# Kernel optimization log

Measured on AMD Instinct MI355X. Metric: run time of the kernel, lower is better.

The kernel has to match this reference:

```python
import jax, jax.numpy as jnp
import numpy as np

D_MODEL = 2048
N_HEADS = 16
HEAD_DIM = D_MODEL // N_HEADS
FF = 8192
KCONV = 4
EPS = 1e-5


def _layernorm(x, w, b, eps=EPS):
    m = jnp.mean(x, axis=-1, keepdims=True)
    v = jnp.mean(jnp.square(x - m), axis=-1, keepdims=True)
    return (x - m) * jax.lax.rsqrt(v + eps) * w + b


def setup_inputs() -> dict:
    key = jax.random.key(0)
    ks = jax.random.split(key, 32)
    B, T = 2, 4096
    s = lambda fan: 1.0 / np.sqrt(fan)
    inp = {
        "x": jax.random.normal(ks[0], (B, T, D_MODEL), jnp.float32),
        # attention projections (stored as [in, out])
        "Wq": jax.random.normal(ks[1], (D_MODEL, D_MODEL), jnp.float32) * s(D_MODEL),
        "Wk": jax.random.normal(ks[2], (D_MODEL, D_MODEL), jnp.float32) * s(D_MODEL),
        "Wv": jax.random.normal(ks[3], (D_MODEL, D_MODEL), jnp.float32) * s(D_MODEL),
        "Wo": jax.random.normal(ks[4], (D_MODEL, D_MODEL), jnp.float32) * s(D_MODEL),
        # depthwise causal conv (torch Conv1d weight layout [C,1,K])
        "conv_w": jax.random.normal(ks[5], (D_MODEL, 1, KCONV), jnp.float32) * s(KCONV),
        "conv_b": jnp.zeros((D_MODEL,), jnp.float32),
        # gates (matching reset_parameters: zero weights, special biases)
        "Wig": jnp.zeros((D_MODEL, D_MODEL), jnp.float32),
        "big": jnp.full((D_MODEL,), -3.0, jnp.float32),
        "Wog": jax.random.normal(ks[6], (D_MODEL, D_MODEL), jnp.float32) * s(D_MODEL),
        "bog": jnp.zeros((D_MODEL,), jnp.float32),
        "Wg": jnp.zeros((D_MODEL, N_HEADS), jnp.float32),
        "bg": jnp.asarray(np.log(
            (lambda d: d / (1.0 - d))(
                1.0 - np.exp(np.linspace(np.log(1 - 0.9), np.log(1 - 0.999), N_HEADS))
            )
        ), jnp.float32),
        # norms
        "vnw": jnp.ones((HEAD_DIM,), jnp.float32),
        "vnb": jnp.zeros((HEAD_DIM,), jnp.float32),
        "mnw": jnp.ones((HEAD_DIM,), jnp.float32),
        "mnb": jnp.zeros((HEAD_DIM,), jnp.float32),
        "gnw": jnp.ones((D_MODEL,), jnp.float32),
        "gnb": jnp.zeros((D_MODEL,), jnp.float32),
        "ln1w": jnp.ones((D_MODEL,), jnp.float32),
        "ln1b": jnp.zeros((D_MODEL,), jnp.float32),
        "ln2w": jnp.ones((D_MODEL,), jnp.float32),
        "ln2b": jnp.zeros((D_MODEL,), jnp.float32),
        # SwiGLU MLP
        "Wgate": jax.random.normal(ks[7], (D_MODEL, FF), jnp.float32) * s(D_MODEL),
        "Wval": jax.random.normal(ks[8], (D_MODEL, FF), jnp.float32) * s(D_MODEL),
        "Wout": jax.random.normal(ks[9], (FF, D_MODEL), jnp.float32) * s(FF),
    }
    return inp


def _long_block(x, Wq, Wk, Wv, Wo, conv_w, conv_b, Wig, big, Wog, bog, Wg, bg,
                vnw, vnb, mnw, mnb, gnw, gnb, ln1w, ln1b, ln2w, ln2b,
                Wgate, Wval, Wout):
    B, T, C = x.shape
    H, D = N_HEADS, HEAD_DIM

    # ---- ln1 + LongAttention ----
    h = _layernorm(x, ln1w, ln1b)

    # depthwise causal conv over time
    ht = jnp.transpose(h, (0, 2, 1))  # [B, C, T]
    xc = jax.lax.conv_general_dilated(
        ht, conv_w, window_strides=(1,), padding=[(KCONV - 1, 0)],
        dimension_numbers=("NCH", "OIH", "NCH"), feature_group_count=C,
    ) + conv_b[None, :, None]
    x_conv = jax.nn.silu(jnp.transpose(xc, (0, 2, 1)))  # [B, T, C]

    def l2norm(t):
        return t * jax.lax.rsqrt(jnp.sum(t * t, axis=-1, keepdims=True) + 1e-12)

    q = l2norm((h @ Wq).reshape(B, T, H, D))
    k = l2norm((h @ Wk).reshape(B, T, H, D))
    v = _layernorm((h @ Wv).reshape(B, T, H, D), vnw, vnb)

    i_gate = jax.nn.sigmoid(x_conv @ Wig + big).reshape(B, T, H, D)
    gamma = jax.nn.sigmoid(x_conv @ Wg + bg).reshape(B, T, H, 1)

    # gated linear-attention recurrence: mem_t = gamma_t * mem_{t-1} + i_t * k_t * v_t
    u = i_gate * k * v
    g = jnp.broadcast_to(gamma, u.shape)

    def combine(c1, c2):
        a1, b1 = c1
        a2, b2 = c2
        return (a1 * a2, a2 * b1 + b2)

    _, mem = jax.lax.associative_scan(combine, (g, u), axis=1)  # [B, T, H, D]

    out = (_layernorm(mem, mnw, mnb) * q).reshape(B, T, C)

    # GroupNorm(num_heads, d_model) applied per token
    og = out.reshape(B, T, H, D)
    m = jnp.mean(og, axis=-1, keepdims=True)
    var = jnp.mean(jnp.square(og - m), axis=-1, keepdims=True)
    og = (og - m) * jax.lax.rsqrt(var + EPS)
    out = (og * gnw.reshape(H, D) + gnb.reshape(H, D)).reshape(B, T, C)

    out = out * jax.nn.sigmoid(x_conv @ Wog + bog)
    h = x + out @ Wo

    # ---- ln2 + SwiGLU MLP ----
    h2 = _layernorm(h, ln2w, ln2b)
    mlp = (jax.nn.silu(h2 @ Wgate) * (h2 @ Wval)) @ Wout
    return h + mlp


def reference(x, Wq, Wk, Wv, Wo, conv_w, conv_b, Wig, big, Wog, bog, Wg, bg,
              vnw, vnb, mnw, mnb, gnw, gnb, ln1w, ln1b, ln2w, ln2b,
              Wgate, Wval, Wout):
    return _long_block(x, Wq, Wk, Wv, Wo, conv_w, conv_b, Wig, big, Wog, bog,
                       Wg, bg, vnw, vnb, mnw, mnb, gnw, gnb, ln1w, ln1b,
                       ln2w, ln2b, Wgate, Wval, Wout)
```

## Files before the change

kernel.cpp:

```cpp
#include <hip/hip_runtime.h>


#define D_MODEL 2048
#define NHEADS 16
#define HEADDIM 128
#define FFDIM 8192
#define BSZ 2
#define TLEN 4096
#define MTOK (BSZ * TLEN)
#define CHUNK 128
#define NCHUNK (TLEN / CHUNK)

typedef unsigned short u16;
typedef __attribute__((ext_vector_type(8))) short bf16x8;
typedef __attribute__((ext_vector_type(4))) float f32x4;

__device__ __forceinline__ float bf2f(unsigned u) {
    u <<= 16;
    float f;
    __builtin_memcpy(&f, &u, 4);
    return f;
}
__device__ __forceinline__ u16 f2bf(float f) {
    unsigned u;
    __builtin_memcpy(&u, &f, 4);
    u = u + 0x7fffu + ((u >> 16) & 1u);
    return (u16)(u >> 16);
}
__device__ __forceinline__ void unpack8(uint4 p, float* v) {
    v[0] = bf2f(p.x & 0xffffu); v[1] = bf2f(p.x >> 16);
    v[2] = bf2f(p.y & 0xffffu); v[3] = bf2f(p.y >> 16);
    v[4] = bf2f(p.z & 0xffffu); v[5] = bf2f(p.z >> 16);
    v[6] = bf2f(p.w & 0xffffu); v[7] = bf2f(p.w >> 16);
}
__device__ __forceinline__ uint4 pack8(const float* v) {
    uint4 p;
    p.x = (unsigned)f2bf(v[0]) | ((unsigned)f2bf(v[1]) << 16);
    p.y = (unsigned)f2bf(v[2]) | ((unsigned)f2bf(v[3]) << 16);
    p.z = (unsigned)f2bf(v[4]) | ((unsigned)f2bf(v[5]) << 16);
    p.w = (unsigned)f2bf(v[6]) | ((unsigned)f2bf(v[7]) << 16);
    return p;
}
__device__ __forceinline__ float sigmoidf_(float x) { return 1.0f / (1.0f + __expf(-x)); }

__device__ __forceinline__ float ld1f(const void* p, size_t i, int f) {
    return f ? ((const float*)p)[i] : bf2f(((const u16*)p)[i]);
}
__device__ __forceinline__ void ld8f(const void* p, size_t i, int f, float* v) {
    if (f) {
        const float4* fp = (const float4*)((const float*)p + i);
        float4 a = fp[0], b = fp[1];
        v[0] = a.x; v[1] = a.y; v[2] = a.z; v[3] = a.w;
        v[4] = b.x; v[5] = b.y; v[6] = b.z; v[7] = b.w;
    } else {
        uint4 q = *(const uint4*)((const u16*)p + i);
        unpack8(q, v);
    }
}

__device__ __forceinline__ void async16(const u16* g, u16* l) {
    __builtin_amdgcn_global_load_lds((const __attribute__((address_space(1))) void*)g,
                                     (__attribute__((address_space(3))) void*)l, 16, 0, 0);
}

__global__ __launch_bounds__(256) void detect_k(const u16* __restrict__ probe, int* __restrict__ flag) {
    int tid = threadIdx.x;
    int cnt = 0;
    for (int i = tid; i < 16384; i += 256) {
        unsigned e = (probe[i] >> 7) & 0xFFu;
        if (e == 0xFFu) cnt++;
    }
#pragma unroll
    for (int off = 32; off; off >>= 1) cnt += __shfl_xor(cnt, off, 64);
    __shared__ int tot[4];
    if ((tid & 63) == 0) tot[tid >> 6] = cnt;
    __syncthreads();
    if (tid == 0) flag[0] = (tot[0] + tot[1] + tot[2] + tot[3] > 4) ? 1 : 0;
}

__global__ void copyflag_k(const int* __restrict__ a, int* __restrict__ b) { b[0] = a[0]; }

__global__ __launch_bounds__(256) void transpose_k(const void* __restrict__ in, u16* __restrict__ out,
                                                   int K, int N, const int* __restrict__ fl) {
    int f = *fl;
    __shared__ u16 tile[32][33];
    int n0 = blockIdx.x * 32, k0 = blockIdx.y * 32;
    int tx = threadIdx.x, ty = threadIdx.y;
#pragma unroll
    for (int j = 0; j < 4; ++j)
        tile[ty + j * 8][tx] = f2bf(ld1f(in, (size_t)(k0 + ty + j * 8) * N + n0 + tx, f));
    __syncthreads();
#pragma unroll
    for (int j = 0; j < 4; ++j)
        out[(size_t)(n0 + ty + j * 8) * K + k0 + tx] = tile[tx][ty + j * 8];
}

template <int IN_RAW>
__global__ __launch_bounds__(256) void ln_rows(const void* __restrict__ in, u16* __restrict__ out,
                                               const void* __restrict__ w, const void* __restrict__ bb,
                                               const int* __restrict__ fl) {
    int f = *fl;
    int m = blockIdx.x, tid = threadIdx.x;
    size_t base = (size_t)m * D_MODEL + tid * 8;
    float v[8];
    ld8f(in, base, IN_RAW ? f : 0, v);
    float s = 0.f, ss = 0.f;
#pragma unroll
    for (int i = 0; i < 8; ++i) { s += v[i]; ss += v[i] * v[i]; }
#pragma unroll
    for (int off = 32; off; off >>= 1) { s += __shfl_xor(s, off, 64); ss += __shfl_xor(ss, off, 64); }
    __shared__ float red[8];
    int lane = tid & 63, wvi = tid >> 6;
    if (lane == 0) { red[wvi] = s; red[4 + wvi] = ss; }
    __syncthreads();
    s = red[0] + red[1] + red[2] + red[3];
    ss = red[4] + red[5] + red[6] + red[7];
    float mu = s * (1.f / D_MODEL);
    float var = ss * (1.f / D_MODEL) - mu * mu;
    float rs = rsqrtf(var + 1e-5f);
    int ci = tid * 8;
    float o[8];
#pragma unroll
    for (int i = 0; i < 8; ++i)
        o[i] = (v[i] - mu) * rs * ld1f(w, ci + i, f) + ld1f(bb, ci + i, f);
    *(uint4*)&out[base] = pack8(o);
}

__global__ __launch_bounds__(256) void conv_silu_k(const u16* __restrict__ h, const void* __restrict__ cw,
                                                   const void* __restrict__ cb, u16* __restrict__ out,
                                                   const int* __restrict__ fl) {
    int f = *fl;
    int m = blockIdx.x, tid = threadIdx.x;
    int b = m >> 12, t = m & (TLEN - 1);
    int c = tid * 8;
    float acc[8];
#pragma unroll
    for (int i = 0; i < 8; ++i) acc[i] = ld1f(cb, c + i, f);
    float wv[8][4];
#pragma unroll
    for (int i = 0; i < 8; ++i) {
        if (f) {
            float4 wp = *(const float4*)((const float*)cw + (size_t)(c + i) * 4);
            wv[i][0] = wp.x; wv[i][1] = wp.y; wv[i][2] = wp.z; wv[i][3] = wp.w;
        } else {
            uint2 wp = *(const uint2*)((const u16*)cw + (size_t)(c + i) * 4);
            wv[i][0] = bf2f(wp.x & 0xffffu); wv[i][1] = bf2f(wp.x >> 16);
            wv[i][2] = bf2f(wp.y & 0xffffu); wv[i][3] = bf2f(wp.y >> 16);
        }
    }
#pragma unroll
    for (int j = 0; j < 4; ++j) {
        int tj = t - 3 + j;
        if (tj < 0) continue;
        uint4 hp = *(const uint4*)&h[((size_t)(b * TLEN + tj)) * D_MODEL + c];
        float hv[8];
        unpack8(hp, hv);
#pragma unroll
        for (int i = 0; i < 8; ++i) acc[i] += wv[i][j] * hv[i];
    }
    float o[8];
#pragma unroll
    for (int i = 0; i < 8; ++i) o[i] = acc[i] * sigmoidf_(acc[i]);
    *(uint4*)&out[(size_t)m * D_MODEL + c] = pack8(o);
}

template <int EPI>
__global__ __launch_bounds__(256) void gemm_bt(const u16* __restrict__ A, const u16* __restrict__ BT,
                                               void* out, const void* aux, const int* fl,
                                               long long oofs, int M, int N, int K) {
    __shared__ u16 As[128 * 32];
    __shared__ u16 Bs[128 * 32];
    const int tid = threadIdx.x;
    const int lane = tid & 63;
    const int wv = tid >> 6;
    const int m0 = blockIdx.y * 128, n0 = blockIdx.x * 128;
    const int wm = (wv >> 1) * 64, wn = (wv & 1) * 64;

    const int c0 = tid, c1 = tid + 256;
    const u16* Ag0 = A + (size_t)(m0 + (c0 >> 2)) * K + ((c0 & 3) * 8);
    const u16* Ag1 = A + (size_t)(m0 + (c1 >> 2)) * K + ((c1 & 3) * 8);
    const u16* Bg0 = BT + (size_t)(n0 + (c0 >> 2)) * K + ((c0 & 3) * 8);
    const u16* Bg1 = BT + (size_t)(n0 + (c1 >> 2)) * K + ((c1 & 3) * 8);
    u16* lA0 = &As[wv * 512];
    u16* lA1 = &As[2048 + wv * 512];
    u16* lB0 = &Bs[wv * 512];
    u16* lB1 = &Bs[2048 + wv * 512];

    f32x4 acc[4][4];
#pragma unroll
    for (int i = 0; i < 4; ++i)
#pragma unroll
        for (int j = 0; j < 4; ++j) acc[i][j] = (f32x4)0.0f;

    const int arow = (lane & 15) * 32 + (lane >> 4) * 8;
    const int kit = K >> 5;
    for (int kt = 0; kt < kit; ++kt) {
        __syncthreads();
        async16(Ag0, lA0);
        async16(Ag1, lA1);
        async16(Bg0, lB0);
        async16(Bg1, lB1);
        Ag0 += 32; Ag1 += 32; Bg0 += 32; Bg1 += 32;
        __syncthreads();
        bf16x8 af[4], bfr[4];
#pragma unroll
        for (int i = 0; i < 4; ++i) af[i] = *(const bf16x8*)&As[(wm + i * 16) * 32 + arow];
#pragma unroll
        for (int j = 0; j < 4; ++j) bfr[j] = *(const bf16x8*)&Bs[(wn + j * 16) * 32 + arow];
#pragma unroll
        for (int i = 0; i < 4; ++i)
#pragma unroll
            for (int j = 0; j < 4; ++j)
                acc[i][j] = __builtin_amdgcn_mfma_f32_16x16x32_bf16(af[i], bfr[j], acc[i][j], 0, 0, 0);
    }

    int f = (EPI == 1 || EPI == 2 || EPI == 4) ? *fl : 0;
    const int col0 = n0 + wn + (lane & 15);
    const int row0 = m0 + wm + ((lane >> 4) << 2);
#pragma unroll
    for (int i = 0; i < 4; ++i) {
#pragma unroll
        for (int r = 0; r < 4; ++r) {
            int row = row0 + i * 16 + r;
            size_t base = (size_t)row * N;
#pragma unroll
            for (int j = 0; j < 4; ++j) {
                int col = col0 + j * 16;
                float v = acc[i][j][r];
                if (EPI == 0) {
                    ((u16*)out)[base + col] = f2bf(v);
                } else if (EPI == 1) {
                    ((u16*)out)[base + col] = f2bf(sigmoidf_(v + ld1f(aux, col, f)));
                } else if (EPI == 2) {
                    ((u16*)out)[base + col] = f2bf(v + ld1f(aux, base + col, f));
                } else if (EPI == 3) {
                    float g = bf2f(((const u16*)aux)[base + col]);
                    ((u16*)out)[base + col] = f2bf(g * sigmoidf_(g) * v);
                } else {
                    float hr = bf2f(((const u16*)aux)[base + col]);
                    if (f) ((float*)out)[oofs + base + col] = v + hr;
                    else   ((u16*)out)[oofs + base + col] = f2bf(v + hr);
                }
            }
        }
    }
}

__global__ __launch_bounds__(256) void l2norm_k(u16* __restrict__ x) {
    int m = blockIdx.x, tid = threadIdx.x;
    size_t base = (size_t)m * D_MODEL + tid * 8;
    uint4 p = *(const uint4*)&x[base];
    float v[8];
    unpack8(p, v);
    float s = 0.f;
#pragma unroll
    for (int i = 0; i < 8; ++i) s += v[i] * v[i];
    s += __shfl_xor(s, 1, 64); s += __shfl_xor(s, 2, 64);
    s += __shfl_xor(s, 4, 64); s += __shfl_xor(s, 8, 64);
    float sc = rsqrtf(s + 1e-12f);
    float o[8];
#pragma unroll
    for (int i = 0; i < 8; ++i) o[i] = v[i] * sc;
    *(uint4*)&x[base] = pack8(o);
}

__global__ __launch_bounds__(256) void vnorm_k(u16* __restrict__ x, const void* __restrict__ w,
                                               const void* __restrict__ bb, const int* __restrict__ fl) {
    int f = *fl;
    int m = blockIdx.x, tid = threadIdx.x;
    size_t base = (size_t)m * D_MODEL + tid * 8;
    uint4 p = *(const uint4*)&x[base];
    float v[8];
    unpack8(p, v);
    float s = 0.f, ss = 0.f;
#pragma unroll
    for (int i = 0; i < 8; ++i) { s += v[i]; ss += v[i] * v[i]; }
    s += __shfl_xor(s, 1, 64); s += __shfl_xor(s, 2, 64);
    s += __shfl_xor(s, 4, 64); s += __shfl_xor(s, 8, 64);
    ss += __shfl_xor(ss, 1, 64); ss += __shfl_xor(ss, 2, 64);
    ss += __shfl_xor(ss, 4, 64); ss += __shfl_xor(ss, 8, 64);
    float mu = s * (1.f / HEADDIM);
    float var = ss * (1.f / HEADDIM) - mu * mu;
    float rs = rsqrtf(var + 1e-5f);
    int d0 = (tid * 8) & 127;
    float o[8];
#pragma unroll
    for (int i = 0; i < 8; ++i) o[i] = (v[i] - mu) * rs * ld1f(w, d0 + i, f) + ld1f(bb, d0 + i, f);
    *(uint4*)&x[base] = pack8(o);
}

__global__ __launch_bounds__(256) void gamma_k(const u16* __restrict__ xc, const void* __restrict__ Wg,
                                               const void* __restrict__ bg, float* __restrict__ gamma,
                                               const int* __restrict__ fl) {
    int f = *fl;
    int m = blockIdx.x, tid = threadIdx.x;
    float g[16];
#pragma unroll
    for (int h = 0; h < 16; ++h) g[h] = 0.f;
    size_t base = (size_t)m * D_MODEL + tid * 8;
    uint4 xp = *(const uint4*)&xc[base];
    float xv[8];
    unpack8(xp, xv);
#pragma unroll
    for (int i = 0; i < 8; ++i) {
        float wv[16];
        size_t ro = (size_t)(tid * 8 + i) * 16;
        if (f) {
            const float4* wr = (const float4*)((const float*)Wg + ro);
#pragma unroll
            for (int q = 0; q < 4; ++q) {
                float4 w4 = wr[q];
                wv[q * 4 + 0] = w4.x; wv[q * 4 + 1] = w4.y; wv[q * 4 + 2] = w4.z; wv[q * 4 + 3] = w4.w;
            }
        } else {
            const u16* wrow = (const u16*)Wg + ro;
            uint4 w0 = *(const uint4*)&wrow[0];
            uint4 w1 = *(const uint4*)&wrow[8];
            unpack8(w0, wv);
            unpack8(w1, wv + 8);
        }
#pragma unroll
        for (int h = 0; h < 16; ++h) g[h] += xv[i] * wv[h];
    }
#pragma unroll
    for (int h = 0; h < 16; ++h)
#pragma unroll
        for (int off = 32; off; off >>= 1) g[h] += __shfl_xor(g[h], off, 64);
    __shared__ float part[4][16];
    int lane = tid & 63, wvi = tid >> 6;
    if (lane == 0)
#pragma unroll
        for (int h = 0; h < 16; ++h) part[wvi][h] = g[h];
    __syncthreads();
    if (tid < 16) {
        float s = part[0][tid] + part[1][tid] + part[2][tid] + part[3][tid] + ld1f(bg, tid, f);
        gamma[(size_t)m * 16 + tid] = sigmoidf_(s);
    }
}

__global__ __launch_bounds__(256) void scan1(const u16* __restrict__ ig, const u16* __restrict__ kn,
                                             const u16* __restrict__ vn, const float* __restrict__ gamma,
                                             float* __restrict__ mem, float* __restrict__ pp) {
    int idx = blockIdx.x;
    int cblk = idx & 7, ch = (idx >> 3) & (NCHUNK - 1), b = idx >> 8;
    int c = cblk * 256 + threadIdx.x;
    int h = c >> 7;
    float mval = 0.f, p = 1.f;
    int t0 = ch * CHUNK;
    size_t rowbase = ((size_t)(b * TLEN + t0)) * D_MODEL + c;
    size_t grow = (size_t)(b * TLEN + t0) * 16 + h;
    bool writepp = ((c & 127) == 0);
    for (int s = 0; s < CHUNK; ++s) {
        float u = bf2f(ig[rowbase]) * bf2f(kn[rowbase]) * bf2f(vn[rowbase]);
        float g = gamma[grow];
        mval = g * mval + u;
        p *= g;
        mem[rowbase] = mval;
        if (writepp) pp[grow] = p;
        rowbase += D_MODEL;
        grow += 16;
    }
}

__global__ __launch_bounds__(256) void scan2(const float* __restrict__ mem, const float* __restrict__ pp,
                                             float* __restrict__ carry) {
    int idx = blockIdx.x * 256 + threadIdx.x;
    int b = idx >> 11, c = idx & 2047, h = c >> 7;
    float cy = 0.f;
    for (int ch = 0; ch < NCHUNK; ++ch) {
        carry[((size_t)(b * NCHUNK + ch)) * D_MODEL + c] = cy;
        int tend = ch * CHUNK + CHUNK - 1;
        float P = pp[((size_t)(b * TLEN + tend)) * 16 + h];
        float le = mem[((size_t)(b * TLEN + tend)) * D_MODEL + c];
        cy = P * cy + le;
    }
}

__global__ __launch_bounds__(256) void attn_epi(const float* __restrict__ mem, const float* __restrict__ pp,
                                                const float* __restrict__ carry, const u16* __restrict__ qn,
                                                const u16* __restrict__ og, const void* __restrict__ mnw,
                                                const void* __restrict__ mnb, const void* __restrict__ gnw,
                                                const void* __restrict__ gnb, u16* __restrict__ outb,
                                                const int* __restrict__ fl) {
    int f = *fl;
    int m = blockIdx.x, tid = threadIdx.x;
    int b = m >> 12, t = m & (TLEN - 1);
    int ch = t >> 7;
    int c = tid * 8, h = c >> 7;
    size_t base = (size_t)m * D_MODEL + c;
    float mv[8];
    {
        const float4* p = (const float4*)&mem[base];
        float4 a = p[0], bb4 = p[1];
        mv[0] = a.x; mv[1] = a.y; mv[2] = a.z; mv[3] = a.w;
        mv[4] = bb4.x; mv[5] = bb4.y; mv[6] = bb4.z; mv[7] = bb4.w;
    }
    float ppv = pp[(size_t)m * 16 + h];
    {
        const float4* p = (const float4*)&carry[((size_t)(b * NCHUNK + ch)) * D_MODEL + c];
        float4 a = p[0], bb4 = p[1];
        mv[0] += ppv * a.x; mv[1] += ppv * a.y; mv[2] += ppv * a.z; mv[3] += ppv * a.w;
        mv[4] += ppv * bb4.x; mv[5] += ppv * bb4.y; mv[6] += ppv * bb4.z; mv[7] += ppv * bb4.w;
    }
    float s = 0.f, ss = 0.f;
#pragma unroll
    for (int i = 0; i < 8; ++i) { s += mv[i]; ss += mv[i] * mv[i]; }
    s += __shfl_xor(s, 1, 64); s += __shfl_xor(s, 2, 64);
    s += __shfl_xor(s, 4, 64); s += __shfl_xor(s, 8, 64);
    ss += __shfl_xor(ss, 1, 64); ss += __shfl_xor(ss, 2, 64);
    ss += __shfl_xor(ss, 4, 64); ss += __shfl_xor(ss, 8, 64);
    float mu = s * (1.f / HEADDIM);
    float var = ss * (1.f / HEADDIM) - mu * mu;
    float rs = rsqrtf(var + 1e-5f);
    int d0 = c & 127;
    uint4 qp = *(const uint4*)&qn[base];
    float qv[8];
    unpack8(qp, qv);
    float o[8];
#pragma unroll
    for (int i = 0; i < 8; ++i)
        o[i] = ((mv[i] - mu) * rs * ld1f(mnw, d0 + i, f) + ld1f(mnb, d0 + i, f)) * qv[i];
    float s2 = 0.f, ss2 = 0.f;
#pragma unroll
    for (int i = 0; i < 8; ++i) { s2 += o[i]; ss2 += o[i] * o[i]; }
    s2 += __shfl_xor(s2, 1, 64); s2 += __shfl_xor(s2, 2, 64);
    s2 += __shfl_xor(s2, 4, 64); s2 += __shfl_xor(s2, 8, 64);
    ss2 += __shfl_xor(ss2, 1, 64); ss2 += __shfl_xor(ss2, 2, 64);
    ss2 += __shfl_xor(ss2, 4, 64); ss2 += __shfl_xor(ss2, 8, 64);
    float mu2 = s2 * (1.f / HEADDIM);
    float var2 = ss2 * (1.f / HEADDIM) - mu2 * mu2;
    float rs2 = rsqrtf(var2 + 1e-5f);
    uint4 ogp = *(const uint4*)&og[base];
    float ogv[8];
    unpack8(ogp, ogv);
    float ob[8];
#pragma unroll
    for (int i = 0; i < 8; ++i)
        ob[i] = ((o[i] - mu2) * rs2 * ld1f(gnw, c + i, f) + ld1f(gnb, c + i, f)) * ogv[i];
    *(uint4*)&outb[base] = pack8(ob);
}

#define SLOT 33554432ull
#define WS_NEED (SLOT * 8)
#define FLAGA_OFF 18350080ull
#define FLAGB_OFF (SLOT * 4)

extern "C" void kernel_launch(void* const* d_in, const int* in_sizes, int n_in,
                              void* d_out, int out_size, void* d_ws, size_t ws_size,
                              hipStream_t stream) {
    if (ws_size < WS_NEED) return;

    const void* x     = d_in[0];
    const void* Wq    = d_in[1];
    const void* Wk    = d_in[2];
    const void* Wv    = d_in[3];
    const void* Wo    = d_in[4];
    const void* convw = d_in[5];
    const void* convb = d_in[6];
    const void* Wig   = d_in[7];
    const void* big   = d_in[8];
    const void* Wog   = d_in[9];
    const void* bog   = d_in[10];
    const void* Wg    = d_in[11];
    const void* bg    = d_in[12];
    const void* vnw   = d_in[13];
    const void* vnb   = d_in[14];
    const void* mnw   = d_in[15];
    const void* mnb   = d_in[16];
    const void* gnw   = d_in[17];
    const void* gnb   = d_in[18];
    const void* ln1w  = d_in[19];
    const void* ln1b  = d_in[20];
    const void* ln2w  = d_in[21];
    const void* ln2b  = d_in[22];
    const void* Wgate = d_in[23];
    const void* Wval  = d_in[24];
    const void* Wout  = d_in[25];

    char* ws = (char*)d_ws;
    u16* wT      = (u16*)(ws);
    float* gamma = (float*)(ws + 16777216);
    float* pp    = (float*)(ws + 16777216 + 524288);
    float* carry = (float*)(ws + 16777216 + 1048576);
    int* flagA   = (int*)(ws + FLAGA_OFF);
    int* flagB   = (int*)(ws + FLAGB_OFF);
    u16* hb      = (u16*)(ws + SLOT * 1);
    u16* xcb     = (u16*)(ws + SLOT * 2);
    float* mem   = (float*)(ws + SLOT * 1);
    u16* wTgate  = (u16*)(ws);
    u16* wTval   = (u16*)(ws + SLOT * 1);
    u16* wTout   = (u16*)(ws + SLOT * 2);
    u16* qn      = (u16*)(ws + SLOT * 3);
    u16* h2b     = (u16*)(ws + SLOT * 3);
    u16* kn      = (u16*)(ws + SLOT * 4);
    u16* attn    = (u16*)(ws + SLOT * 4);
    u16* vn      = (u16*)(ws + SLOT * 5);
    u16* hres    = (u16*)(ws + SLOT * 5);
    u16* ig      = (u16*)(ws + SLOT * 6);
    u16* og      = (u16*)(ws + SLOT * 7);
    u16* graw    = (u16*)(ws + SLOT * 6);

    dim3 tb(32, 8);

    detect_k<<<1, 256, 0, stream>>>((const u16*)x, flagA);

    ln_rows<1><<<MTOK, 256, 0, stream>>>(x, hb, ln1w, ln1b, flagA);
    conv_silu_k<<<MTOK, 256, 0, stream>>>(hb, convw, convb, xcb, flagA);

    transpose_k<<<dim3(64, 64), tb, 0, stream>>>(Wq, wT, 2048, 2048, flagA);
    gemm_bt<0><<<dim3(16, 64), 256, 0, stream>>>(hb, wT, qn, nullptr, nullptr, 0, MTOK, 2048, 2048);
    transpose_k<<<dim3(64, 64), tb, 0, stream>>>(Wk, wT, 2048, 2048, flagA);
    gemm_bt<0><<<dim3(16, 64), 256, 0, stream>>>(hb, wT, kn, nullptr, nullptr, 0, MTOK, 2048, 2048);
    transpose_k<<<dim3(64, 64), tb, 0, stream>>>(Wv, wT, 2048, 2048, flagA);
    gemm_bt<0><<<dim3(16, 64), 256, 0, stream>>>(hb, wT, vn, nullptr, nullptr, 0, MTOK, 2048, 2048);
    l2norm_k<<<MTOK, 256, 0, stream>>>(qn);
    l2norm_k<<<MTOK, 256, 0, stream>>>(kn);
    vnorm_k<<<MTOK, 256, 0, stream>>>(vn, vnw, vnb, flagA);

    transpose_k<<<dim3(64, 64), tb, 0, stream>>>(Wig, wT, 2048, 2048, flagA);
    gemm_bt<1><<<dim3(16, 64), 256, 0, stream>>>(xcb, wT, ig, big, flagA, 0, MTOK, 2048, 2048);
    transpose_k<<<dim3(64, 64), tb, 0, stream>>>(Wog, wT, 2048, 2048, flagA);
    gemm_bt<1><<<dim3(16, 64), 256, 0, stream>>>(xcb, wT, og, bog, flagA, 0, MTOK, 2048, 2048);
    gamma_k<<<MTOK, 256, 0, stream>>>(xcb, Wg, bg, gamma, flagA);

    scan1<<<BSZ * NCHUNK * 8, 256, 0, stream>>>(ig, kn, vn, gamma, mem, pp);
    scan2<<<16, 256, 0, stream>>>(mem, pp, carry);
    attn_epi<<<MTOK, 256, 0, stream>>>(mem, pp, carry, qn, og, mnw, mnb, gnw, gnb, attn, flagA);

    transpose_k<<<dim3(64, 64), tb, 0, stream>>>(Wo, wT, 2048, 2048, flagA);
    gemm_bt<2><<<dim3(16, 64), 256, 0, stream>>>(attn, wT, hres, x, flagA, 0, MTOK, 2048, 2048);
    ln_rows<0><<<MTOK, 256, 0, stream>>>(hres, h2b, ln2w, ln2b, flagA);

    copyflag_k<<<1, 1, 0, stream>>>(flagA, flagB);

    transpose_k<<<dim3(256, 64), tb, 0, stream>>>(Wgate, wTgate, 2048, 8192, flagB);
    transpose_k<<<dim3(256, 64), tb, 0, stream>>>(Wval, wTval, 2048, 8192, flagB);
    transpose_k<<<dim3(64, 256), tb, 0, stream>>>(Wout, wTout, 8192, 2048, flagB);

    for (int half = 0; half < 2; ++half) {
        const u16* a2 = h2b + (size_t)half * 4096 * 2048;
        const u16* hr = hres + (size_t)half * 4096 * 2048;
        long long oofs = (long long)half * 4096 * 2048;
        gemm_bt<0><<<dim3(64, 32), 256, 0, stream>>>(a2, wTgate, graw, nullptr, nullptr, 0, 4096, 8192, 2048);
        gemm_bt<3><<<dim3(64, 32), 256, 0, stream>>>(a2, wTval, graw, graw, nullptr, 0, 4096, 8192, 2048);
        gemm_bt<4><<<dim3(16, 32), 256, 0, stream>>>(graw, wTout, d_out, hr, flagB, oofs, 4096, 2048, 8192);
    }
}
```

Baseline: 3.024 ms.

## Replace 128x128 GEMM with 256x256 double-buffered swizzled-LDS MFMA kernel

Replaces the simple 128x128-tile GEMM, which synchronises twice per 32-wide K step, with a 512-thread 256x256-tile kernel. The new kernel uses a 64-wide K step, double-buffered LDS with XOR swizzling, and interleaves async global-to-LDS prefetch with MFMA groups under explicit s_barrier/vmcnt waits and setprio. The larger tile raises arithmetic intensity, and the prefetch is meant to hide load latency. It uses 128KB of LDS and many accumulators per wave, so occupancy and correctness depend on the hand-written barrier schedule.

```diff
diff --git a/kernel.cpp b/kernel.cpp
--- a/kernel.cpp
+++ b/kernel.cpp
@@ -165,60 +165,159 @@
 }
 
 template <int EPI>
-__global__ __launch_bounds__(256) void gemm_bt(const u16* __restrict__ A, const u16* __restrict__ BT,
-                                               void* out, const void* aux, const int* fl,
-                                               long long oofs, int M, int N, int K) {
-    __shared__ u16 As[128 * 32];
-    __shared__ u16 Bs[128 * 32];
+__global__ __launch_bounds__(512, 2) void gemm256(const u16* __restrict__ A, const u16* __restrict__ BT,
+                                                  void* out, const void* aux, const int* fl,
+                                                  long long oofs, int M, int N, int K) {
+    __shared__ u16 As[2][16384];
+    __shared__ u16 Bs[2][16384];
     const int tid = threadIdx.x;
     const int lane = tid & 63;
     const int wv = tid >> 6;
-    const int m0 = blockIdx.y * 128, n0 = blockIdx.x * 128;
-    const int wm = (wv >> 1) * 64, wn = (wv & 1) * 64;
-
-    const int c0 = tid, c1 = tid + 256;
-    const u16* Ag0 = A + (size_t)(m0 + (c0 >> 2)) * K + ((c0 & 3) * 8);
-    const u16* Ag1 = A + (size_t)(m0 + (c1 >> 2)) * K + ((c1 & 3) * 8);
-    const u16* Bg0 = BT + (size_t)(n0 + (c0 >> 2)) * K + ((c0 & 3) * 8);
-    const u16* Bg1 = BT + (size_t)(n0 + (c1 >> 2)) * K + ((c1 & 3) * 8);
-    u16* lA0 = &As[wv * 512];
-    u16* lA1 = &As[2048 + wv * 512];
-    u16* lB0 = &Bs[wv * 512];
-    u16* lB1 = &Bs[2048 + wv * 512];
-
-    f32x4 acc[4][4];
-#pragma unroll
-    for (int i = 0; i < 4; ++i)
+    const int wm = wv >> 2;
+    const int wn = wv & 3;
+    const int m0 = blockIdx.y * 256, n0 = blockIdx.x * 256;
+
+    const int r0 = tid >> 3;
+    const int cS = ((tid & 7) << 3) ^ ((r0 & 4) << 2);
+    const u16* aB = A + (size_t)(m0 + r0) * K + cS;
+    const u16* bB = BT + (size_t)(n0 + r0) * K + cS;
+
+    const int fr = lane & 15;
+    const int kq = (lane >> 4) << 3;
+    const int sw = (fr & 4) << 2;
+    const int rdA0 = (wm * 128 + fr) * 64 + (kq ^ sw);
+    const int rdA1 = (wm * 128 + fr) * 64 + ((32 + kq) ^ sw);
+    const int rdB0 = (wn * 64 + fr) * 64 + (kq ^ sw);
+    const int rdB1 = (wn * 64 + fr) * 64 + ((32 + kq) ^ sw);
+
+    f32x4 acc[8][4];
+#pragma unroll
+    for (int i = 0; i < 8; ++i)
 #pragma unroll
         for (int j = 0; j < 4; ++j) acc[i][j] = (f32x4)0.0f;
 
-    const int arow = (lane & 15) * 32 + (lane >> 4) * 8;
-    const int kit = K >> 5;
-    for (int kt = 0; kt < kit; ++kt) {
-        __syncthreads();
-        async16(Ag0, lA0);
-        async16(Ag1, lA1);
-        async16(Bg0, lB0);
-        async16(Bg1, lB1);
-        Ag0 += 32; Ag1 += 32; Bg0 += 32; Bg1 += 32;
-        __syncthreads();
-        bf16x8 af[4], bfr[4];
-#pragma unroll
-        for (int i = 0; i < 4; ++i) af[i] = *(const bf16x8*)&As[(wm + i * 16) * 32 + arow];
-#pragma unroll
-        for (int j = 0; j < 4; ++j) bfr[j] = *(const bf16x8*)&Bs[(wn + j * 16) * 32 + arow];
-#pragma unroll
-        for (int i = 0; i < 4; ++i)
-#pragma unroll
-            for (int j = 0; j < 4; ++j)
-                acc[i][j] = __builtin_amdgcn_mfma_f32_16x16x32_bf16(af[i], bfr[j], acc[i][j], 0, 0, 0);
-    }
+    bf16x8 a[4][2], b0[2][2], b1[2][2];
+
+#define BARX() asm volatile("s_barrier" ::: "memory")
+#define WAITV(n) asm volatile("s_waitcnt vmcnt(" #n ")" ::: "memory")
+#define STG_A(sel, h, tI)                                                                        \
+    do {                                                                                         \
+        async16(aB + (size_t)((h) * 128) * K + (size_t)(tI) * 64,                                \
+                &As[sel][(h) * 8192 + (tid >> 6) * 512]);                                        \
+        async16(aB + (size_t)((h) * 128 + 64) * K + (size_t)(tI) * 64,                           \
+                &As[sel][(h) * 8192 + 4096 + (tid >> 6) * 512]);                                 \
+    } while (0)
+#define STG_B(sel, h, tI)                                                                        \
+    do {                                                                                         \
+        async16(bB + (size_t)((h) * 128) * K + (size_t)(tI) * 64,                                \
+                &Bs[sel][(h) * 8192 + (tid >> 6) * 512]);                                        \
+        async16(bB + (size_t)((h) * 128 + 64) * K + (size_t)(tI) * 64,                           \
+                &Bs[sel][(h) * 8192 + 4096 + (tid >> 6) * 512]);                                 \
+    } while (0)
+#define LDA4(s, base)                                                                            \
+    do {                                                                                         \
+        a[0][0] = *(const bf16x8*)&As[s][rdA0 + (base + 0) * 1024];                              \
+        a[0][1] = *(const bf16x8*)&As[s][rdA1 + (base + 0) * 1024];                              \
+        a[1][0] = *(const bf16x8*)&As[s][rdA0 + (base + 1) * 1024];                              \
+        a[1][1] = *(const bf16x8*)&As[s][rdA1 + (base + 1) * 1024];                              \
+        a[2][0] = *(const bf16x8*)&As[s][rdA0 + (base + 2) * 1024];                              \
+        a[2][1] = *(const bf16x8*)&As[s][rdA1 + (base + 2) * 1024];                              \
+        a[3][0] = *(const bf16x8*)&As[s][rdA0 + (base + 3) * 1024];                              \
+        a[3][1] = *(const bf16x8*)&As[s][rdA1 + (base + 3) * 1024];                              \
+    } while (0)
+#define LDB2(s, base, bb)                                                                        \
+    do {                                                                                         \
+        bb[0][0] = *(const bf16x8*)&Bs[s][rdB0 + (base + 0) * 1024];                             \
+        bb[0][1] = *(const bf16x8*)&Bs[s][rdB1 + (base + 0) * 1024];                             \
+        bb[1][0] = *(const bf16x8*)&Bs[s][rdB0 + (base + 1) * 1024];                             \
+        bb[1][1] = *(const bf16x8*)&Bs[s][rdB1 + (base + 1) * 1024];                             \
+    } while (0)
+#define MM8(I0, J0, bb)                                                                          \
+    do {                                                                                         \
+        __builtin_amdgcn_s_setprio(1);                                                           \
+        _Pragma("unroll") for (int i_ = 0; i_ < 4; ++i_) {                                       \
+            _Pragma("unroll") for (int j_ = 0; j_ < 2; ++j_) {                                   \
+                acc[(I0) + i_][(J0) + j_] = __builtin_amdgcn_mfma_f32_16x16x32_bf16(             \
+                    a[i_][0], bb[j_][0], acc[(I0) + i_][(J0) + j_], 0, 0, 0);                    \
+                acc[(I0) + i_][(J0) + j_] = __builtin_amdgcn_mfma_f32_16x16x32_bf16(             \
+                    a[i_][1], bb[j_][1], acc[(I0) + i_][(J0) + j_], 0, 0, 0);                    \
+            }                                                                                    \
+        }                                                                                        \
+        __builtin_amdgcn_s_setprio(0);                                                           \
+    } while (0)
+
+    STG_A(0, 0, 0);
+    STG_A(0, 1, 0);
+    STG_B(0, 0, 0);
+    STG_B(0, 1, 0);
+    STG_B(1, 0, 1);
+    STG_B(1, 1, 1);
+    WAITV(4);
+    BARX();
+
+    const int NT = K >> 6;
+    for (int t = 0; t < NT; t += 2) {
+        const int tn = t + 1;
+        const int t2 = (t + 2 < NT) ? t + 2 : NT - 1;
+        const int t3 = (t + 3 < NT) ? t + 3 : NT - 1;
+        LDA4(0, 0);
+        LDB2(0, 0, b0);
+        STG_A(1, 0, tn);
+        BARX();
+        MM8(0, 0, b0);
+        BARX();
+        LDB2(0, 2, b1);
+        STG_A(1, 1, tn);
+        BARX();
+        MM8(0, 2, b1);
+        BARX();
+        LDA4(0, 4);
+        STG_B(0, 0, t2);
+        BARX();
+        MM8(4, 0, b0);
+        BARX();
+        STG_B(0, 1, t2);
+        BARX();
+        MM8(4, 2, b1);
+        WAITV(4);
+        BARX();
+        LDA4(1, 0);
+        LDB2(1, 0, b0);
+        STG_A(0, 0, t2);
+        BARX();
+        MM8(0, 0, b0);
+        BARX();
+        LDB2(1, 2, b1);
+        STG_A(0, 1, t2);
+        BARX();
+        MM8(0, 2, b1);
+        BARX();
+        LDA4(1, 4);
+        STG_B(1, 0, t3);
+        BARX();
+        MM8(4, 0, b0);
+        BARX();
+        STG_B(1, 1, t3);
+        BARX();
+        MM8(4, 2, b1);
+        WAITV(4);
+        BARX();
+    }
+    WAITV(0);
+
+#undef BARX
+#undef WAITV
+#undef STG_A
+#undef STG_B
+#undef LDA4
+#undef LDB2
+#undef MM8
 
     int f = (EPI == 1 || EPI == 2 || EPI == 4) ? *fl : 0;
-    const int col0 = n0 + wn + (lane & 15);
-    const int row0 = m0 + wm + ((lane >> 4) << 2);
-#pragma unroll
-    for (int i = 0; i < 4; ++i) {
+    const int col0 = n0 + wn * 64 + (lane & 15);
+    const int row0 = m0 + wm * 128 + ((lane >> 4) << 2);
+#pragma unroll
+    for (int i = 0; i < 8; ++i) {
 #pragma unroll
         for (int r = 0; r < 4; ++r) {
             int row = row0 + i * 16 + r;
@@ -508,19 +607,19 @@
     conv_silu_k<<<MTOK, 256, 0, stream>>>(hb, convw, convb, xcb, flagA);
 
     transpose_k<<<dim3(64, 64), tb, 0, stream>>>(Wq, wT, 2048, 2048, flagA);
-    gemm_bt<0><<<dim3(16, 64), 256, 0, stream>>>(hb, wT, qn, nullptr, nullptr, 0, MTOK, 2048, 2048);
+    gemm256<0><<<dim3(8, 32), 512, 0, stream>>>(hb, wT, qn, nullptr, nullptr, 0, MTOK, 2048, 2048);
     transpose_k<<<dim3(64, 64), tb, 0, stream>>>(Wk, wT, 2048, 2048, flagA);
-    gemm_bt<0><<<dim3(16, 64), 256, 0, stream>>>(hb, wT, kn, nullptr, nullptr, 0, MTOK, 2048, 2048);
+    gemm256<0><<<dim3(8, 32), 512, 0, stream>>>(hb, wT, kn, nullptr, nullptr, 0, MTOK, 2048, 2048);
     transpose_k<<<dim3(64, 64), tb, 0, stream>>>(Wv, wT, 2048, 2048, flagA);
-    gemm_bt<0><<<dim3(16, 64), 256, 0, stream>>>(hb, wT, vn, nullptr, nullptr, 0, MTOK, 2048, 2048);
+    gemm256<0><<<dim3(8, 32), 512, 0, stream>>>(hb, wT, vn, nullptr, nullptr, 0, MTOK, 2048, 2048);
     l2norm_k<<<MTOK, 256, 0, stream>>>(qn);
     l2norm_k<<<MTOK, 256, 0, stream>>>(kn);
     vnorm_k<<<MTOK, 256, 0, stream>>>(vn, vnw, vnb, flagA);
 
     transpose_k<<<dim3(64, 64), tb, 0, stream>>>(Wig, wT, 2048, 2048, flagA);
-    gemm_bt<1><<<dim3(16, 64), 256, 0, stream>>>(xcb, wT, ig, big, flagA, 0, MTOK, 2048, 2048);
+    gemm256<1><<<dim3(8, 32), 512, 0, stream>>>(xcb, wT, ig, big, flagA, 0, MTOK, 2048, 2048);
     transpose_k<<<dim3(64, 64), tb, 0, stream>>>(Wog, wT, 2048, 2048, flagA);
-    gemm_bt<1><<<dim3(16, 64), 256, 0, stream>>>(xcb, wT, og, bog, flagA, 0, MTOK, 2048, 2048);
+    gemm256<1><<<dim3(8, 32), 512, 0, stream>>>(xcb, wT, og, bog, flagA, 0, MTOK, 2048, 2048);
     gamma_k<<<MTOK, 256, 0, stream>>>(xcb, Wg, bg, gamma, flagA);
 
     scan1<<<BSZ * NCHUNK * 8, 256, 0, stream>>>(ig, kn, vn, gamma, mem, pp);
@@ -528,7 +627,7 @@
     attn_epi<<<MTOK, 256, 0, stream>>>(mem, pp, carry, qn, og, mnw, mnb, gnw, gnb, attn, flagA);
 
     transpose_k<<<dim3(64, 64), tb, 0, stream>>>(Wo, wT, 2048, 2048, flagA);
-    gemm_bt<2><<<dim3(16, 64), 256, 0, stream>>>(attn, wT, hres, x, flagA, 0, MTOK, 2048, 2048);
+    gemm256<2><<<dim3(8, 32), 512, 0, stream>>>(attn, wT, hres, x, flagA, 0, MTOK, 2048, 2048);
     ln_rows<0><<<MTOK, 256, 0, stream>>>(hres, h2b, ln2w, ln2b, flagA);
 
     copyflag_k<<<1, 1, 0, stream>>>(flagA, flagB);
@@ -541,8 +640,8 @@
         const u16* a2 = h2b + (size_t)half * 4096 * 2048;
         const u16* hr = hres + (size_t)half * 4096 * 2048;
         long long oofs = (long long)half * 4096 * 2048;
-        gemm_bt<0><<<dim3(64, 32), 256, 0, stream>>>(a2, wTgate, graw, nullptr, nullptr, 0, 4096, 8192, 2048);
-        gemm_bt<3><<<dim3(64, 32), 256, 0, stream>>>(a2, wTval, graw, graw, nullptr, 0, 4096, 8192, 2048);
-        gemm_bt<4><<<dim3(16, 32), 256, 0, stream>>>(graw, wTout, d_out, hr, flagB, oofs, 4096, 2048, 8192);
-    }
-}
+        gemm256<0><<<dim3(32, 16), 512, 0, stream>>>(a2, wTgate, graw, nullptr, nullptr, 0, 4096, 8192, 2048);
+        gemm256<3><<<dim3(32, 16), 512, 0, stream>>>(a2, wTval, graw, graw, nullptr, 0, 4096, 8192, 2048);
+        gemm256<4><<<dim3(8, 16), 512, 0, stream>>>(graw, wTout, d_out, hr, flagB, oofs, 4096, 2048, 8192);
+    }
+}
```

Result: faster. 2.751 ms (-9.0%).

## Double-buffer GEMM LDS tiles with swizzled layout and XCD-aware block remap

Applied to the files above, without the earlier changes.

Rewrites the bf16 MFMA GEMM to double-buffer its LDS tiles, so the next K-slice's async global-to-LDS loads overlap the current slice's MFMAs, with one barrier per iteration instead of two. It also XOR-swizzles the LDS column layout to cut bank conflicts, remaps block indices so neighbouring tiles share an XCD for better L2 reuse, raises wave priority around the MFMA block and sets a minimum-occupancy launch bound. Doubling LDS to 32KB per block could limit occupancy, and the remap assumes grid x is a multiple of 8.

```diff
diff --git a/kernel.cpp b/kernel.cpp
--- a/kernel.cpp
+++ b/kernel.cpp
@@ -165,26 +165,35 @@
 }
 
 template <int EPI>
-__global__ __launch_bounds__(256) void gemm_bt(const u16* __restrict__ A, const u16* __restrict__ BT,
-                                               void* out, const void* aux, const int* fl,
-                                               long long oofs, int M, int N, int K) {
-    __shared__ u16 As[128 * 32];
-    __shared__ u16 Bs[128 * 32];
+__global__ __launch_bounds__(256, 4) void gemmT(const u16* __restrict__ A, const u16* __restrict__ BT,
+                                                void* out, const void* aux, const int* fl,
+                                                long long oofs, int M, int N, int K) {
+    __shared__ u16 As[2][4096];
+    __shared__ u16 Bs[2][4096];
     const int tid = threadIdx.x;
     const int lane = tid & 63;
     const int wv = tid >> 6;
-    const int m0 = blockIdx.y * 128, n0 = blockIdx.x * 128;
-    const int wm = (wv >> 1) * 64, wn = (wv & 1) * 64;
-
-    const int c0 = tid, c1 = tid + 256;
-    const u16* Ag0 = A + (size_t)(m0 + (c0 >> 2)) * K + ((c0 & 3) * 8);
-    const u16* Ag1 = A + (size_t)(m0 + (c1 >> 2)) * K + ((c1 & 3) * 8);
-    const u16* Bg0 = BT + (size_t)(n0 + (c0 >> 2)) * K + ((c0 & 3) * 8);
-    const u16* Bg1 = BT + (size_t)(n0 + (c1 >> 2)) * K + ((c1 & 3) * 8);
-    u16* lA0 = &As[wv * 512];
-    u16* lA1 = &As[2048 + wv * 512];
-    u16* lB0 = &Bs[wv * 512];
-    u16* lB1 = &Bs[2048 + wv * 512];
+    const int wm = wv >> 1;
+    const int wn = wv & 1;
+
+    const int gx = gridDim.x, gy = gridDim.y;
+    const int flat = blockIdx.y * gx + blockIdx.x;
+    const int nxs = gx >> 3;
+    const int xcd = flat & 7, pos = flat >> 3;
+    const int bx = xcd * nxs + pos / gy;
+    const int by = pos % gy;
+    const int m0 = by * 128, n0 = bx * 128;
+
+    const int rS = tid >> 2;
+    const int cS = (((tid & 3) ^ ((tid >> 3) & 3)) << 3);
+    const u16* aB = A + (size_t)(m0 + rS) * K + cS;
+    const u16* bB = BT + (size_t)(n0 + rS) * K + cS;
+
+    const int fr = lane & 15;
+    const int kq = lane >> 4;
+    const int sA = ((kq ^ ((fr >> 1) & 3)) << 3);
+    const int rdA = (wm * 64 + fr) * 32 + sA;
+    const int rdB = (wn * 64 + fr) * 32 + sA;
 
     f32x4 acc[4][4];
 #pragma unroll
@@ -192,31 +201,53 @@
 #pragma unroll
         for (int j = 0; j < 4; ++j) acc[i][j] = (f32x4)0.0f;
 
-    const int arow = (lane & 15) * 32 + (lane >> 4) * 8;
-    const int kit = K >> 5;
-    for (int kt = 0; kt < kit; ++kt) {
-        __syncthreads();
-        async16(Ag0, lA0);
-        async16(Ag1, lA1);
-        async16(Bg0, lB0);
-        async16(Bg1, lB1);
-        Ag0 += 32; Ag1 += 32; Bg0 += 32; Bg1 += 32;
-        __syncthreads();
-        bf16x8 af[4], bfr[4];
-#pragma unroll
-        for (int i = 0; i < 4; ++i) af[i] = *(const bf16x8*)&As[(wm + i * 16) * 32 + arow];
-#pragma unroll
-        for (int j = 0; j < 4; ++j) bfr[j] = *(const bf16x8*)&Bs[(wn + j * 16) * 32 + arow];
+#define BARX() asm volatile("s_barrier" ::: "memory")
+#define WAITV0() asm volatile("s_waitcnt vmcnt(0)" ::: "memory")
+#define STG(sel, tI)                                                                     \
+    do {                                                                                 \
+        const u16* ag_ = aB + (size_t)(tI) * 32;                                         \
+        const u16* bg_ = bB + (size_t)(tI) * 32;                                         \
+        async16(ag_, &As[sel][tid * 8]);                                                 \
+        async16(ag_ + (size_t)64 * K, &As[sel][2048 + tid * 8]);                         \
+        async16(bg_, &Bs[sel][tid * 8]);                                                 \
+        async16(bg_ + (size_t)64 * K, &Bs[sel][2048 + tid * 8]);                         \
+    } while (0)
+
+    STG(0, 0);
+    WAITV0();
+    BARX();
+
+    const int NT = K >> 5;
+    int cur = 0;
+    for (int t = 0; t < NT; ++t) {
+        if (t + 1 < NT) {
+            if (cur) STG(0, t + 1);
+            else     STG(1, t + 1);
+        }
+        bf16x8 a[4], b[4];
+#pragma unroll
+        for (int m = 0; m < 4; ++m) a[m] = *(const bf16x8*)&As[cur][rdA + m * 512];
+#pragma unroll
+        for (int n = 0; n < 4; ++n) b[n] = *(const bf16x8*)&Bs[cur][rdB + n * 512];
+        __builtin_amdgcn_s_setprio(1);
 #pragma unroll
         for (int i = 0; i < 4; ++i)
 #pragma unroll
             for (int j = 0; j < 4; ++j)
-                acc[i][j] = __builtin_amdgcn_mfma_f32_16x16x32_bf16(af[i], bfr[j], acc[i][j], 0, 0, 0);
-    }
+                acc[i][j] = __builtin_amdgcn_mfma_f32_16x16x32_bf16(a[i], b[j], acc[i][j], 0, 0, 0);
+        __builtin_amdgcn_s_setprio(0);
+        WAITV0();
+        BARX();
+        cur ^= 1;
+    }
+
+#undef BARX
+#undef WAITV0
+#undef STG
 
     int f = (EPI == 1 || EPI == 2 || EPI == 4) ? *fl : 0;
-    const int col0 = n0 + wn + (lane & 15);
-    const int row0 = m0 + wm + ((lane >> 4) << 2);
+    const int col0 = n0 + wn * 64 + (lane & 15);
+    const int row0 = m0 + wm * 64 + ((lane >> 4) << 2);
 #pragma unroll
     for (int i = 0; i < 4; ++i) {
 #pragma unroll
@@ -508,19 +539,19 @@
     conv_silu_k<<<MTOK, 256, 0, stream>>>(hb, convw, convb, xcb, flagA);
 
     transpose_k<<<dim3(64, 64), tb, 0, stream>>>(Wq, wT, 2048, 2048, flagA);
-    gemm_bt<0><<<dim3(16, 64), 256, 0, stream>>>(hb, wT, qn, nullptr, nullptr, 0, MTOK, 2048, 2048);
+    gemmT<0><<<dim3(16, 64), 256, 0, stream>>>(hb, wT, qn, nullptr, nullptr, 0, MTOK, 2048, 2048);
     transpose_k<<<dim3(64, 64), tb, 0, stream>>>(Wk, wT, 2048, 2048, flagA);
-    gemm_bt<0><<<dim3(16, 64), 256, 0, stream>>>(hb, wT, kn, nullptr, nullptr, 0, MTOK, 2048, 2048);
+    gemmT<0><<<dim3(16, 64), 256, 0, stream>>>(hb, wT, kn, nullptr, nullptr, 0, MTOK, 2048, 2048);
     transpose_k<<<dim3(64, 64), tb, 0, stream>>>(Wv, wT, 2048, 2048, flagA);
-    gemm_bt<0><<<dim3(16, 64), 256, 0, stream>>>(hb, wT, vn, nullptr, nullptr, 0, MTOK, 2048, 2048);
+    gemmT<0><<<dim3(16, 64), 256, 0, stream>>>(hb, wT, vn, nullptr, nullptr, 0, MTOK, 2048, 2048);
     l2norm_k<<<MTOK, 256, 0, stream>>>(qn);
     l2norm_k<<<MTOK, 256, 0, stream>>>(kn);
     vnorm_k<<<MTOK, 256, 0, stream>>>(vn, vnw, vnb, flagA);
 
     transpose_k<<<dim3(64, 64), tb, 0, stream>>>(Wig, wT, 2048, 2048, flagA);
-    gemm_bt<1><<<dim3(16, 64), 256, 0, stream>>>(xcb, wT, ig, big, flagA, 0, MTOK, 2048, 2048);
+    gemmT<1><<<dim3(16, 64), 256, 0, stream>>>(xcb, wT, ig, big, flagA, 0, MTOK, 2048, 2048);
     transpose_k<<<dim3(64, 64), tb, 0, stream>>>(Wog, wT, 2048, 2048, flagA);
-    gemm_bt<1><<<dim3(16, 64), 256, 0, stream>>>(xcb, wT, og, bog, flagA, 0, MTOK, 2048, 2048);
+    gemmT<1><<<dim3(16, 64), 256, 0, stream>>>(xcb, wT, og, bog, flagA, 0, MTOK, 2048, 2048);
     gamma_k<<<MTOK, 256, 0, stream>>>(xcb, Wg, bg, gamma, flagA);
 
     scan1<<<BSZ * NCHUNK * 8, 256, 0, stream>>>(ig, kn, vn, gamma, mem, pp);
@@ -528,7 +559,7 @@
     attn_epi<<<MTOK, 256, 0, stream>>>(mem, pp, carry, qn, og, mnw, mnb, gnw, gnb, attn, flagA);
 
     transpose_k<<<dim3(64, 64), tb, 0, stream>>>(Wo, wT, 2048, 2048, flagA);
-    gemm_bt<2><<<dim3(16, 64), 256, 0, stream>>>(attn, wT, hres, x, flagA, 0, MTOK, 2048, 2048);
+    gemmT<2><<<dim3(16, 64), 256, 0, stream>>>(attn, wT, hres, x, flagA, 0, MTOK, 2048, 2048);
     ln_rows<0><<<MTOK, 256, 0, stream>>>(hres, h2b, ln2w, ln2b, flagA);
 
     copyflag_k<<<1, 1, 0, stream>>>(flagA, flagB);
@@ -541,8 +572,8 @@
         const u16* a2 = h2b + (size_t)half * 4096 * 2048;
         const u16* hr = hres + (size_t)half * 4096 * 2048;
         long long oofs = (long long)half * 4096 * 2048;
-        gemm_bt<0><<<dim3(64, 32), 256, 0, stream>>>(a2, wTgate, graw, nullptr, nullptr, 0, 4096, 8192, 2048);
-        gemm_bt<3><<<dim3(64, 32), 256, 0, stream>>>(a2, wTval, graw, graw, nullptr, 0, 4096, 8192, 2048);
-        gemm_bt<4><<<dim3(16, 32), 256, 0, stream>>>(graw, wTout, d_out, hr, flagB, oofs, 4096, 2048, 8192);
-    }
-}
+        gemmT<0><<<dim3(64, 32), 256, 0, stream>>>(a2, wTgate, graw, nullptr, nullptr, 0, 4096, 8192, 2048);
+        gemmT<3><<<dim3(64, 32), 256, 0, stream>>>(a2, wTval, graw, graw, nullptr, 0, 4096, 8192, 2048);
+        gemmT<4><<<dim3(16, 32), 256, 0, stream>>>(graw, wTout, d_out, hr, flagB, oofs, 4096, 2048, 8192);
+    }
+}
```

After: 2.732 ms. -9.6%, faster.
